# Kernel tuning notes

Hardware: AMD Instinct MI355X
Metric: run time of the kernel (lower is better)

Reference implementation:

```python
import jax, jax.numpy as jnp
import numpy as np
import math

B, T, C = 4, 2048, 1024
NH, D = 16, 64  # n_head, head_dim; NH * D == C


def setup_inputs() -> dict:
    key = jax.random.key(0)
    ks = jax.random.split(key, 7)
    std = 0.02
    return {
        "x": jax.random.normal(ks[0], (B, T, C), dtype=jnp.float32),
        "W_attn": jax.random.normal(ks[1], (C, 3 * C), dtype=jnp.float32) * std,
        "b_attn": jax.random.normal(ks[2], (3 * C,), dtype=jnp.float32) * std,
        "bQ": jax.random.normal(ks[3], (NH, D), dtype=jnp.float32) * 0.1 + 0.5,
        "bK": jax.random.normal(ks[4], (NH, D), dtype=jnp.float32) * 0.1 + 0.3,
        "W_proj": jax.random.normal(ks[5], (C, C), dtype=jnp.float32) * std,
        "b_proj": jax.random.normal(ks[6], (C,), dtype=jnp.float32) * std,
    }


def reference(x, W_attn, b_attn, bQ, bK, W_proj, b_proj):
    Bx, Tx, Cx = x.shape
    qkv = x @ W_attn + b_attn                      # [B, T, 3C]
    q, k, v = jnp.split(qkv, 3, axis=2)
    # [B, T, C] -> [B, NH, T, D]
    q = q.reshape(Bx, Tx, NH, D).transpose(0, 2, 1, 3)
    k = k.reshape(Bx, Tx, NH, D).transpose(0, 2, 1, 3)
    v = v.reshape(Bx, Tx, NH, D).transpose(0, 2, 1, 3)
    # per-head disorder bias added to Q and K before the dot product
    q = q + bQ[None, :, None, :]
    k = k + bK[None, :, None, :]
    scores = jnp.einsum('bhqd,bhkd->bhqk', q, k) / math.sqrt(D)  # [B, NH, T, T]
    causal = jnp.tril(jnp.ones((Tx, Tx), dtype=bool))
    scores = jnp.where(causal[None, None], scores, jnp.float32(-jnp.inf))
    att = jax.nn.softmax(scores, axis=-1)
    y = jnp.einsum('bhqk,bhkd->bhqd', att, v)      # [B, NH, T, D]
    y = y.transpose(0, 2, 1, 3).reshape(Bx, Tx, Cx)
    return y @ W_proj + b_proj
```

## Files before the change

### kernel.cpp

```cpp
#include <hip/hip_runtime.h>

typedef unsigned short u16;
typedef unsigned int u32;
typedef __bf16 bf16x8 __attribute__((ext_vector_type(8)));
typedef float f32x4 __attribute__((ext_vector_type(4)));

#define B_  4
#define T_  2048
#define C_  1024
#define NH_ 16
#define D_  64
#define M_  (B_*T_)
#define N_QKV (3*C_)

#define ATTN_BLOCKS 1024

#define BARRIER()  __asm__ __volatile__("s_barrier" ::: "memory")
#define WAIT_VM4() __asm__ __volatile__("s_waitcnt vmcnt(4)" ::: "memory")
#define WAIT_VM0() __asm__ __volatile__("s_waitcnt vmcnt(0)" ::: "memory")

__device__ __forceinline__ void async_copy16(void* lds, const void* gptr) {
  __builtin_amdgcn_global_load_lds(
      (const __attribute__((address_space(1))) u32*)gptr,
      (__attribute__((address_space(3))) u32*)(u32)(uintptr_t)lds,
      16, 0, 0);
}

__device__ __forceinline__ u16 f2bf(float f) {
  union { float f; unsigned u; } c; c.f = f;
  unsigned u = c.u;
  unsigned r = (u + 0x7fffu + ((u >> 16) & 1u)) >> 16;
  return (u16)r;
}

__global__ __launch_bounds__(256) void conv_bf16(const float* __restrict__ in,
                                                 u16* __restrict__ out, int n) {
  int i = (blockIdx.x * 256 + threadIdx.x) * 4;
  if (i < n) {
    float4 f = *reinterpret_cast<const float4*>(in + i);
    u16 o[4] = { f2bf(f.x), f2bf(f.y), f2bf(f.z), f2bf(f.w) };
    *reinterpret_cast<uint2*>(out + i) = *reinterpret_cast<uint2*>(o);
  }
}

__global__ __launch_bounds__(256) void transpose_bf16(const float* __restrict__ in,
                                                      u16* __restrict__ out,
                                                      int K, int N) {
  __shared__ float tile[32][33];
  int bi = blockIdx.y;
  int bj = blockIdx.x;
  int tx = threadIdx.x & 31;
  int ty = threadIdx.x >> 5;
#pragma unroll
  for (int i = 0; i < 4; ++i) {
    int row = ty + i * 8;
    tile[row][tx] = in[(bi * 32 + row) * N + bj * 32 + tx];
  }
  __syncthreads();
#pragma unroll
  for (int i = 0; i < 4; ++i) {
    int row = ty + i * 8;
    out[(bj * 32 + row) * K + bi * 32 + tx] = f2bf(tile[tx][row]);
  }
}

__global__ __launch_bounds__(256) void gemm_qkv(const u16* __restrict__ A,
                                                const u16* __restrict__ Bt,
                                                const float* __restrict__ b_attn,
                                                const float* __restrict__ bQ,
                                                const float* __restrict__ bK,
                                                u16* __restrict__ qo,
                                                u16* __restrict__ ko,
                                                u16* __restrict__ vo) {
  const int K = C_;
  int bm = blockIdx.y, bn = blockIdx.x;
  int tid = threadIdx.x;
  int wid = tid >> 6, lane = tid & 63;
  int lm = lane & 15, lq = lane >> 4;
  int wm = (wid >> 1) * 64, wn = (wid & 1) * 64;

  __shared__ u16 As[128 * 32];
  __shared__ u16 Bs[128 * 32];

  f32x4 acc[4][4];
#pragma unroll
  for (int i = 0; i < 4; ++i)
#pragma unroll
    for (int j = 0; j < 4; ++j) acc[i][j] = (f32x4){0.f, 0.f, 0.f, 0.f};

  const u16* Ab = A + (bm * 128) * K;
  const u16* Bb = Bt + (bn * 128) * K;
  int srow = lane >> 2;
  int scol = (lane & 3) * 8;

  for (int k0 = 0; k0 < K; k0 += 32) {
    __syncthreads();
#pragma unroll
    for (int j = 0; j < 2; ++j) {
      int c = wid * 2 + j;
      int row = c * 16 + srow;
      async_copy16(&As[c * 512], Ab + row * K + k0 + scol);
      async_copy16(&Bs[c * 512], Bb + row * K + k0 + scol);
    }
    __syncthreads();
    bf16x8 af[4], bf[4];
#pragma unroll
    for (int mt = 0; mt < 4; ++mt)
      af[mt] = *reinterpret_cast<const bf16x8*>(&As[(wm + mt * 16 + lm) * 32 + lq * 8]);
#pragma unroll
    for (int nt = 0; nt < 4; ++nt)
      bf[nt] = *reinterpret_cast<const bf16x8*>(&Bs[(wn + nt * 16 + lm) * 32 + lq * 8]);
#pragma unroll
    for (int mt = 0; mt < 4; ++mt)
#pragma unroll
      for (int nt = 0; nt < 4; ++nt)
        acc[mt][nt] = __builtin_amdgcn_mfma_f32_16x16x32_bf16(af[mt], bf[nt], acc[mt][nt], 0, 0, 0);
  }

  const float qscale = 0.18033688011112042f;
#pragma unroll
  for (int mt = 0; mt < 4; ++mt) {
#pragma unroll
    for (int nt = 0; nt < 4; ++nt) {
#pragma unroll
      for (int r = 0; r < 4; ++r) {
        int m = bm * 128 + wm + mt * 16 + lq * 4 + r;
        int n = bn * 128 + wn + nt * 16 + lm;
        float val = acc[mt][nt][r] + b_attn[n];
        int sel = n >> 10;
        int c = n & 1023;
        int h = c >> 6;
        int d = c & 63;
        int b = m >> 11;
        int t = m & 2047;
        if (sel == 0)      qo[(((b * NH_ + h) * T_) + t) * D_ + d] = f2bf((val + bQ[c]) * qscale);
        else if (sel == 1) ko[(((b * NH_ + h) * T_) + t) * D_ + d] = f2bf(val + bK[c]);
        else               vo[(((b * NH_ + h) * D_) + d) * T_ + t] = f2bf(val);
      }
    }
  }
}

__global__ __launch_bounds__(256, 4) void attn_kernel(const u16* __restrict__ q,
                                                      const u16* __restrict__ k,
                                                      const u16* __restrict__ vt,
                                                      u16* __restrict__ y) {
  int tid = threadIdx.x;
  int w = tid >> 6, lane = tid & 63;
  int lm = lane & 15, lq = lane >> 4;

  __shared__ u16 Ks[2][64 * 64];
  __shared__ u16 Vs[2][64 * 64];

  int srow = lane >> 3;
  int sg   = (lane & 7) ^ srow;

  int idx = blockIdx.x;
  int c8 = idx & 255, jq = idx >> 8;
  int a = c8 & 7, gq = c8 >> 3;
  int qt, bh;
  if (jq == 0)      { qt = 15 - a; bh = gq; }
  else if (jq == 1) { qt = 8 + a;  bh = 32 + gq; }
  else if (jq == 2) { qt = 7 - a;  bh = gq; }
  else              { qt = a;      bh = 32 + gq; }

  int b = bh >> 4, h = bh & 15;
  const int klast = 2 * qt + 1;
  const int qrow0 = qt * 128 + w * 32;

  const u16* qb = q + ((size_t)bh * T_ + qrow0) * D_;
  const u16* kb = k + (size_t)bh * T_ * D_;
  const u16* vb = vt + (size_t)bh * D_ * T_;

  auto stage_K = [&](int buf, int kbi) {
    const u16* gb = kb + (size_t)(kbi * 64) * 64;
#pragma unroll
    for (int j = 0; j < 2; ++j) {
      int c = w * 2 + j;
      async_copy16(&Ks[buf][c * 512], gb + (c * 8 + srow) * 64 + sg * 8);
    }
  };
  auto stage_V = [&](int buf, int kbi) {
    const u16* gb = vb + kbi * 64;
#pragma unroll
    for (int j = 0; j < 2; ++j) {
      int c = w * 2 + j;
      async_copy16(&Vs[buf][c * 512], gb + (size_t)(c * 8 + srow) * T_ + sg * 8);
    }
  };

  bf16x8 bq[2][2];
#pragma unroll
  for (int qt2 = 0; qt2 < 2; ++qt2) {
    const u16* qp = qb + (qt2 * 16 + lm) * D_ + lq * 8;
    bq[qt2][0] = *reinterpret_cast<const bf16x8*>(qp);
    bq[qt2][1] = *reinterpret_cast<const bf16x8*>(qp + 32);
  }

  f32x4 o[4][2];
#pragma unroll
  for (int dt = 0; dt < 4; ++dt)
#pragma unroll
    for (int qt2 = 0; qt2 < 2; ++qt2) o[dt][qt2] = (f32x4){0.f, 0.f, 0.f, 0.f};
  float mprev[2] = {-1e30f, -1e30f}, lsum[2] = {0.f, 0.f};

  stage_K(0, 0); stage_V(0, 0);
  stage_K(1, 1); stage_V(1, 1);

  for (int kbi = 0; kbi <= klast; ++kbi) {
    int buf = kbi & 1;
    WAIT_VM4();
    BARRIER();

    bf16x8 kf[4][2];
#pragma unroll
    for (int kt = 0; kt < 4; ++kt) {
      const u16* base = &Ks[buf][(kt * 16 + lm) * 64];
      kf[kt][0] = *reinterpret_cast<const bf16x8*>(base + ((lq ^ (lm & 7)) * 8));
      kf[kt][1] = *reinterpret_cast<const bf16x8*>(base + (((4 + lq) ^ (lm & 7)) * 8));
    }

    f32x4 s[4][2];
#pragma unroll
    for (int kt = 0; kt < 4; ++kt)
#pragma unroll
      for (int qt2 = 0; qt2 < 2; ++qt2) {
        f32x4 z = (f32x4){0.f, 0.f, 0.f, 0.f};
        z = __builtin_amdgcn_mfma_f32_16x16x32_bf16(kf[kt][0], bq[qt2][0], z, 0, 0, 0);
        z = __builtin_amdgcn_mfma_f32_16x16x32_bf16(kf[kt][1], bq[qt2][1], z, 0, 0, 0);
        s[kt][qt2] = z;
      }

    bool maskt = (kbi * 64 + 63 > qrow0);
    bf16x8 pb[2][2];
#pragma unroll
    for (int qt2 = 0; qt2 < 2; ++qt2) {
      int qg = qrow0 + qt2 * 16 + lm;
      if (maskt) {
#pragma unroll
        for (int kt = 0; kt < 4; ++kt)
#pragma unroll
          for (int r = 0; r < 4; ++r) {
            int key = kbi * 64 + kt * 16 + lq * 4 + r;
            if (key > qg) s[kt][qt2][r] = -1e30f;
          }
      }
      float mx[4];
#pragma unroll
      for (int kt = 0; kt < 4; ++kt)
        mx[kt] = fmaxf(fmaxf(s[kt][qt2][0], s[kt][qt2][1]),
                       fmaxf(s[kt][qt2][2], s[kt][qt2][3]));
      float mval = fmaxf(fmaxf(mx[0], mx[1]), fmaxf(mx[2], mx[3]));
      mval = fmaxf(mval, __shfl_xor(mval, 16));
      mval = fmaxf(mval, __shfl_xor(mval, 32));
      float mold = mprev[qt2];
      float mnew = fmaxf(mold, mval);
      unsigned long long upd = __ballot(mval > mold);
      if (upd) {
        float alpha = __builtin_exp2f(mold - mnew);
        lsum[qt2] *= alpha;
#pragma unroll
        for (int dt = 0; dt < 4; ++dt) o[dt][qt2] *= alpha;
        mprev[qt2] = mnew;
      }
      float rs = 0.f;
      unsigned pw[8];
#pragma unroll
      for (int kt = 0; kt < 4; ++kt) {
        unsigned pu[4];
#pragma unroll
        for (int r = 0; r < 4; ++r) {
          float p = __builtin_exp2f(s[kt][qt2][r] - mnew);
          rs += p;
          union { float f; unsigned u; } cc; cc.f = p;
          pu[r] = cc.u;
        }
        pw[kt * 2]     = __builtin_amdgcn_perm(pu[1], pu[0], 0x07060302u);
        pw[kt * 2 + 1] = __builtin_amdgcn_perm(pu[3], pu[2], 0x07060302u);
      }
      rs += __shfl_xor(rs, 16);
      rs += __shfl_xor(rs, 32);
      lsum[qt2] += rs;
      union { unsigned u[4]; bf16x8 v; } b0, b1;
#pragma unroll
      for (int t = 0; t < 4; ++t) { b0.u[t] = pw[t]; b1.u[t] = pw[4 + t]; }
      pb[qt2][0] = b0.v;
      pb[qt2][1] = b1.v;
    }

    {
      int r7 = lm & 7;
      int h4 = (lq & 1) * 4;
      int g0 = lq >> 1;
#pragma unroll
      for (int dt = 0; dt < 4; ++dt) {
        const u16* vbase = &Vs[buf][(dt * 16 + lm) * 64];
        union { unsigned long long qd[2]; bf16x8 v; } t0, t1;
        t0.qd[0] = *reinterpret_cast<const unsigned long long*>(vbase + ((g0 ^ r7) * 8) + h4);
        t0.qd[1] = *reinterpret_cast<const unsigned long long*>(vbase + (((g0 + 2) ^ r7) * 8) + h4);
        t1.qd[0] = *reinterpret_cast<const unsigned long long*>(vbase + (((g0 + 4) ^ r7) * 8) + h4);
        t1.qd[1] = *reinterpret_cast<const unsigned long long*>(vbase + (((g0 + 6) ^ r7) * 8) + h4);
#pragma unroll
        for (int qt2 = 0; qt2 < 2; ++qt2) {
          o[dt][qt2] = __builtin_amdgcn_mfma_f32_16x16x32_bf16(t0.v, pb[qt2][0], o[dt][qt2], 0, 0, 0);
          o[dt][qt2] = __builtin_amdgcn_mfma_f32_16x16x32_bf16(t1.v, pb[qt2][1], o[dt][qt2], 0, 0, 0);
        }
      }
    }

    BARRIER();
    int nk = (kbi + 2 <= klast) ? kbi + 2 : klast;
    stage_K(buf, nk); stage_V(buf, nk);
  }

  WAIT_VM0();

#pragma unroll
  for (int qt2 = 0; qt2 < 2; ++qt2) {
    float inv = 1.f / lsum[qt2];
    int qg = qrow0 + qt2 * 16 + lm;
#pragma unroll
    for (int dt = 0; dt < 4; ++dt) {
      u16 wb[4];
#pragma unroll
      for (int r = 0; r < 4; ++r) wb[r] = f2bf(o[dt][qt2][r] * inv);
      int d = dt * 16 + lq * 4;
      *reinterpret_cast<uint2*>(&y[((size_t)(b * T_ + qg) * NH_ + h) * D_ + d]) =
          *reinterpret_cast<uint2*>(wb);
    }
  }
}

__global__ __launch_bounds__(256) void gemm_proj(const u16* __restrict__ A,
                                                 const u16* __restrict__ Bt,
                                                 const float* __restrict__ b_proj,
                                                 float* __restrict__ out) {
  const int K = C_, N = C_;
  int bm = blockIdx.y, bn = blockIdx.x;
  int tid = threadIdx.x;
  int wid = tid >> 6, lane = tid & 63;
  int lm = lane & 15, lq = lane >> 4;
  int wm = (wid >> 1) * 64, wn = (wid & 1) * 64;

  __shared__ u16 As[128 * 32];
  __shared__ u16 Bs[128 * 32];

  f32x4 acc[4][4];
#pragma unroll
  for (int i = 0; i < 4; ++i)
#pragma unroll
    for (int j = 0; j < 4; ++j) acc[i][j] = (f32x4){0.f, 0.f, 0.f, 0.f};

  const u16* Ab = A + (bm * 128) * K;
  const u16* Bb = Bt + (bn * 128) * K;
  int srow = lane >> 2;
  int scol = (lane & 3) * 8;

  for (int k0 = 0; k0 < K; k0 += 32) {
    __syncthreads();
#pragma unroll
    for (int j = 0; j < 2; ++j) {
      int c = wid * 2 + j;
      int row = c * 16 + srow;
      async_copy16(&As[c * 512], Ab + row * K + k0 + scol);
      async_copy16(&Bs[c * 512], Bb + row * K + k0 + scol);
    }
    __syncthreads();
    bf16x8 af[4], bf[4];
#pragma unroll
    for (int mt = 0; mt < 4; ++mt)
      af[mt] = *reinterpret_cast<const bf16x8*>(&As[(wm + mt * 16 + lm) * 32 + lq * 8]);
#pragma unroll
    for (int nt = 0; nt < 4; ++nt)
      bf[nt] = *reinterpret_cast<const bf16x8*>(&Bs[(wn + nt * 16 + lm) * 32 + lq * 8]);
#pragma unroll
    for (int mt = 0; mt < 4; ++mt)
#pragma unroll
      for (int nt = 0; nt < 4; ++nt)
        acc[mt][nt] = __builtin_amdgcn_mfma_f32_16x16x32_bf16(af[mt], bf[nt], acc[mt][nt], 0, 0, 0);
  }

#pragma unroll
  for (int mt = 0; mt < 4; ++mt) {
#pragma unroll
    for (int nt = 0; nt < 4; ++nt) {
#pragma unroll
      for (int r = 0; r < 4; ++r) {
        int m = bm * 128 + wm + mt * 16 + lq * 4 + r;
        int n = bn * 128 + wn + nt * 16 + lm;
        out[m * N + n] = acc[mt][nt][r] + b_proj[n];
      }
    }
  }
}

extern "C" void kernel_launch(void* const* d_in, const int* in_sizes, int n_in,
                              void* d_out, int out_size, void* d_ws, size_t ws_size,
                              hipStream_t stream) {
  const float* x      = (const float*)d_in[0];
  const float* W_attn = (const float*)d_in[1];
  const float* b_attn = (const float*)d_in[2];
  const float* bQ     = (const float*)d_in[3];
  const float* bK     = (const float*)d_in[4];
  const float* W_proj = (const float*)d_in[5];
  const float* b_proj = (const float*)d_in[6];
  float* out = (float*)d_out;

  char* ws = (char*)d_ws;
  u16* xb  = (u16*)(ws);
  u16* WaT = (u16*)(ws + 16777216);
  u16* WpT = (u16*)(ws + 23068672);
  u16* qw  = (u16*)(ws + 25165824);
  u16* kw  = (u16*)(ws + 41943040);
  u16* vw  = (u16*)(ws + 58720256);
  u16* yw  = (u16*)(ws + 75497472);

  conv_bf16<<<M_ * C_ / (4 * 256), 256, 0, stream>>>(x, xb, M_ * C_);
  {
    dim3 g(N_QKV / 32, C_ / 32);
    transpose_bf16<<<g, 256, 0, stream>>>(W_attn, WaT, C_, N_QKV);
  }
  {
    dim3 g(C_ / 32, C_ / 32);
    transpose_bf16<<<g, 256, 0, stream>>>(W_proj, WpT, C_, C_);
  }
  {
    dim3 g(N_QKV / 128, M_ / 128);
    gemm_qkv<<<g, 256, 0, stream>>>(xb, WaT, b_attn, bQ, bK, qw, kw, vw);
  }
  attn_kernel<<<ATTN_BLOCKS, 256, 0, stream>>>(qw, kw, vw, yw);
  {
    dim3 g(C_ / 128, M_ / 128);
    gemm_proj<<<g, 256, 0, stream>>>(yw, WpT, b_proj, out);
  }
}
```

Measured before the change: 317.0 us.

## Rewrite QKV GEMM as 256x256 double-buffered pipelined tile; double-buffer proj GEMM

Rebuilds the QKV projection GEMM around 256x256 output tiles with 512 threads, a K-step of 64, XOR-swizzled LDS layout, double-buffered async global-to-LDS loads interleaved with MFMA quads, s_setprio hints, and an XCD-aware block remap. It also vectorizes the V-transpose stores. The output projection GEMM gets a simple double-buffered prefetch that replaces its two syncthreads per K-step. The aim is to hide global load latency and raise MFMA utilization, at the cost of much larger LDS use (128KB for QKV), heavier register pressure, and fragile manual waitcnt and barrier ordering.

```diff
diff --git a/kernel.cpp b/kernel.cpp
--- a/kernel.cpp
+++ b/kernel.cpp
@@ -18,6 +18,7 @@
 #define BARRIER()  __asm__ __volatile__("s_barrier" ::: "memory")
 #define WAIT_VM4() __asm__ __volatile__("s_waitcnt vmcnt(4)" ::: "memory")
 #define WAIT_VM0() __asm__ __volatile__("s_waitcnt vmcnt(0)" ::: "memory")
+#define LGKM0()    __asm__ __volatile__("s_waitcnt lgkmcnt(0)" ::: "memory")
 
 __device__ __forceinline__ void async_copy16(void* lds, const void* gptr) {
   __builtin_amdgcn_global_load_lds(
@@ -64,78 +65,151 @@
   }
 }
 
-__global__ __launch_bounds__(256) void gemm_qkv(const u16* __restrict__ A,
-                                                const u16* __restrict__ Bt,
-                                                const float* __restrict__ b_attn,
-                                                const float* __restrict__ bQ,
-                                                const float* __restrict__ bK,
-                                                u16* __restrict__ qo,
-                                                u16* __restrict__ ko,
-                                                u16* __restrict__ vo) {
+__global__ __launch_bounds__(512, 2) void gemm_qkv(const u16* __restrict__ A,
+                                                   const u16* __restrict__ Bt,
+                                                   const float* __restrict__ b_attn,
+                                                   const float* __restrict__ bQ,
+                                                   const float* __restrict__ bK,
+                                                   u16* __restrict__ qo,
+                                                   u16* __restrict__ ko,
+                                                   u16* __restrict__ vo) {
   const int K = C_;
-  int bm = blockIdx.y, bn = blockIdx.x;
+  const int NT = K / 64;
+  int bid = blockIdx.x;
+  int wg = (bid & 7) * 48 + (bid >> 3);
+  int bm = wg / 12, bn = wg % 12;
+
   int tid = threadIdx.x;
-  int wid = tid >> 6, lane = tid & 63;
+  int w = tid >> 6, lane = tid & 63;
   int lm = lane & 15, lq = lane >> 4;
-  int wm = (wid >> 1) * 64, wn = (wid & 1) * 64;
-
-  __shared__ u16 As[128 * 32];
-  __shared__ u16 Bs[128 * 32];
-
-  f32x4 acc[4][4];
-#pragma unroll
-  for (int i = 0; i < 4; ++i)
+  int wr = w >> 2, wc = w & 3;
+
+  __shared__ u16 As[2][256 * 64];
+  __shared__ u16 Bs[2][256 * 64];
+
+  const u16* Ab = A + (size_t)(bm * 256) * K;
+  const u16* Bb = Bt + (size_t)(bn * 256) * K;
+  int srow = lane >> 3;
+  int sgc  = ((lane & 7) ^ srow) * 8;
+
+  auto stageA = [&](int bb, int h, int t) {
+#pragma unroll
+    for (int j = 0; j < 2; ++j)
+      async_copy16(&As[bb][h * 8192 + j * 4096 + w * 512],
+                   Ab + (size_t)(h * 128 + j * 64 + w * 8 + srow) * K + t * 64 + sgc);
+  };
+  auto stageB = [&](int bb, int h, int t) {
+#pragma unroll
+    for (int j = 0; j < 2; ++j)
+      async_copy16(&Bs[bb][h * 8192 + j * 4096 + w * 512],
+                   Bb + (size_t)(h * 128 + j * 64 + w * 8 + srow) * K + t * 64 + sgc);
+  };
+
+  f32x4 acc[8][4];
+#pragma unroll
+  for (int i = 0; i < 8; ++i)
 #pragma unroll
     for (int j = 0; j < 4; ++j) acc[i][j] = (f32x4){0.f, 0.f, 0.f, 0.f};
 
-  const u16* Ab = A + (bm * 128) * K;
-  const u16* Bb = Bt + (bn * 128) * K;
-  int srow = lane >> 2;
-  int scol = (lane & 3) * 8;
-
-  for (int k0 = 0; k0 < K; k0 += 32) {
-    __syncthreads();
-#pragma unroll
-    for (int j = 0; j < 2; ++j) {
-      int c = wid * 2 + j;
-      int row = c * 16 + srow;
-      async_copy16(&As[c * 512], Ab + row * K + k0 + scol);
-      async_copy16(&Bs[c * 512], Bb + row * K + k0 + scol);
-    }
-    __syncthreads();
-    bf16x8 af[4], bf[4];
-#pragma unroll
-    for (int mt = 0; mt < 4; ++mt)
-      af[mt] = *reinterpret_cast<const bf16x8*>(&As[(wm + mt * 16 + lm) * 32 + lq * 8]);
-#pragma unroll
-    for (int nt = 0; nt < 4; ++nt)
-      bf[nt] = *reinterpret_cast<const bf16x8*>(&Bs[(wn + nt * 16 + lm) * 32 + lq * 8]);
-#pragma unroll
-    for (int mt = 0; mt < 4; ++mt)
-#pragma unroll
-      for (int nt = 0; nt < 4; ++nt)
-        acc[mt][nt] = __builtin_amdgcn_mfma_f32_16x16x32_bf16(af[mt], bf[nt], acc[mt][nt], 0, 0, 0);
-  }
+  auto readA4 = [&](bf16x8 (&af)[4][2], int bb, int mh) {
+#pragma unroll
+    for (int mf = 0; mf < 4; ++mf) {
+      const u16* base = &As[bb][(wr * 128 + (mh * 4 + mf) * 16 + lm) * 64];
+#pragma unroll
+      for (int kh = 0; kh < 2; ++kh)
+        af[mf][kh] = *reinterpret_cast<const bf16x8*>(base + (((kh * 4 + lq) ^ (lm & 7)) * 8));
+    }
+  };
+  auto readB8 = [&](bf16x8 (&bf)[4][2], int bb) {
+#pragma unroll
+    for (int nf = 0; nf < 4; ++nf) {
+      const u16* base = &Bs[bb][(wc * 64 + nf * 16 + lm) * 64];
+#pragma unroll
+      for (int kh = 0; kh < 2; ++kh)
+        bf[nf][kh] = *reinterpret_cast<const bf16x8*>(base + (((kh * 4 + lq) ^ (lm & 7)) * 8));
+    }
+  };
+  auto quad = [&](bf16x8 (&af)[4][2], bf16x8 (&bf)[4][2], int mb, int nb) {
+#pragma unroll
+    for (int mf = 0; mf < 4; ++mf)
+#pragma unroll
+      for (int nf = 0; nf < 2; ++nf)
+#pragma unroll
+        for (int kh = 0; kh < 2; ++kh)
+          acc[mb + mf][nb + nf] = __builtin_amdgcn_mfma_f32_16x16x32_bf16(
+              af[mf][kh], bf[nb + nf][kh], acc[mb + mf][nb + nf], 0, 0, 0);
+  };
+
+  auto process = [&](int bb, int tbx, int bbx, int tay, int bay) {
+    bf16x8 bfr[4][2], aflo[4][2], afhi[4][2];
+    readB8(bfr, bb);
+    readA4(aflo, bb, 0);
+    stageB(bbx, 0, tbx);
+    BARRIER(); LGKM0();
+    __builtin_amdgcn_s_setprio(1); quad(aflo, bfr, 0, 0); __builtin_amdgcn_s_setprio(0);
+    BARRIER();
+    readA4(afhi, bb, 1);
+    stageB(bbx, 1, tbx);
+    BARRIER(); LGKM0();
+    __builtin_amdgcn_s_setprio(1); quad(aflo, bfr, 0, 2); __builtin_amdgcn_s_setprio(0);
+    BARRIER();
+    stageA(bay, 0, tay);
+    BARRIER();
+    __builtin_amdgcn_s_setprio(1); quad(afhi, bfr, 4, 0); __builtin_amdgcn_s_setprio(0);
+    BARRIER();
+    stageA(bay, 1, tay);
+    WAIT_VM4();
+    BARRIER();
+    __builtin_amdgcn_s_setprio(1); quad(afhi, bfr, 4, 2); __builtin_amdgcn_s_setprio(0);
+    BARRIER();
+  };
+
+  stageA(0, 0, 0); stageA(0, 1, 0); stageB(0, 0, 0); stageB(0, 1, 0);
+  stageA(1, 0, 1); stageA(1, 1, 1);
+  WAIT_VM4();
+  BARRIER();
+
+  for (int i = 0; i < NT / 2; ++i) {
+    int t0 = 2 * i, t1 = t0 + 1;
+    int s2 = (t0 + 2 < NT) ? t0 + 2 : NT - 1;
+    int s3 = (t0 + 3 < NT) ? t0 + 3 : NT - 1;
+    process(0, t1, 1, s2, 0);
+    process(1, s2, 0, s3, 1);
+  }
+  WAIT_VM0();
 
   const float qscale = 0.18033688011112042f;
-#pragma unroll
-  for (int mt = 0; mt < 4; ++mt) {
-#pragma unroll
-    for (int nt = 0; nt < 4; ++nt) {
-#pragma unroll
-      for (int r = 0; r < 4; ++r) {
-        int m = bm * 128 + wm + mt * 16 + lq * 4 + r;
-        int n = bn * 128 + wn + nt * 16 + lm;
-        float val = acc[mt][nt][r] + b_attn[n];
-        int sel = n >> 10;
-        int c = n & 1023;
-        int h = c >> 6;
-        int d = c & 63;
-        int b = m >> 11;
-        int t = m & 2047;
-        if (sel == 0)      qo[(((b * NH_ + h) * T_) + t) * D_ + d] = f2bf((val + bQ[c]) * qscale);
-        else if (sel == 1) ko[(((b * NH_ + h) * T_) + t) * D_ + d] = f2bf(val + bK[c]);
-        else               vo[(((b * NH_ + h) * D_) + d) * T_ + t] = f2bf(val);
+  int sel = bn >> 2;
+#pragma unroll
+  for (int mf = 0; mf < 8; ++mf) {
+#pragma unroll
+    for (int nf = 0; nf < 4; ++nf) {
+      int n = bn * 256 + wc * 64 + nf * 16 + lm;
+      float bias = b_attn[n];
+      int c = n & 1023;
+      int h = c >> 6;
+      int d = c & 63;
+      int m0 = bm * 256 + wr * 128 + mf * 16 + lq * 4;
+      int b = m0 >> 11;
+      int t = m0 & 2047;
+      if (sel == 0) {
+        float qb = bQ[c];
+#pragma unroll
+        for (int r = 0; r < 4; ++r)
+          qo[(((size_t)(b * NH_ + h) * T_) + t + r) * D_ + d] =
+              f2bf((acc[mf][nf][r] + bias + qb) * qscale);
+      } else if (sel == 1) {
+        float kb2 = bK[c];
+#pragma unroll
+        for (int r = 0; r < 4; ++r)
+          ko[(((size_t)(b * NH_ + h) * T_) + t + r) * D_ + d] =
+              f2bf(acc[mf][nf][r] + bias + kb2);
+      } else {
+        u16 wb[4];
+#pragma unroll
+        for (int r = 0; r < 4; ++r) wb[r] = f2bf(acc[mf][nf][r] + bias);
+        *reinterpret_cast<uint2*>(&vo[((size_t)(b * NH_ + h) * D_ + d) * T_ + t]) =
+            *reinterpret_cast<uint2*>(wb);
       }
     }
   }
@@ -342,8 +416,8 @@
   int lm = lane & 15, lq = lane >> 4;
   int wm = (wid >> 1) * 64, wn = (wid & 1) * 64;
 
-  __shared__ u16 As[128 * 32];
-  __shared__ u16 Bs[128 * 32];
+  __shared__ u16 As[2][128 * 32];
+  __shared__ u16 Bs[2][128 * 32];
 
   f32x4 acc[4][4];
 #pragma unroll
@@ -356,29 +430,40 @@
   int srow = lane >> 2;
   int scol = (lane & 3) * 8;
 
-  for (int k0 = 0; k0 < K; k0 += 32) {
-    __syncthreads();
+  auto stage = [&](int bb, int k0) {
 #pragma unroll
     for (int j = 0; j < 2; ++j) {
       int c = wid * 2 + j;
       int row = c * 16 + srow;
-      async_copy16(&As[c * 512], Ab + row * K + k0 + scol);
-      async_copy16(&Bs[c * 512], Bb + row * K + k0 + scol);
-    }
-    __syncthreads();
+      async_copy16(&As[bb][c * 512], Ab + row * K + k0 + scol);
+      async_copy16(&Bs[bb][c * 512], Bb + row * K + k0 + scol);
+    }
+  };
+
+  stage(0, 0);
+  const int NTp = K / 32;
+  for (int t = 0; t < NTp; ++t) {
+    int bb = t & 1;
+    int k1 = (t + 1 < NTp) ? (t + 1) * 32 : t * 32;
+    stage(bb ^ 1, k1);
+    WAIT_VM4();
+    BARRIER();
     bf16x8 af[4], bf[4];
 #pragma unroll
     for (int mt = 0; mt < 4; ++mt)
-      af[mt] = *reinterpret_cast<const bf16x8*>(&As[(wm + mt * 16 + lm) * 32 + lq * 8]);
+      af[mt] = *reinterpret_cast<const bf16x8*>(&As[bb][(wm + mt * 16 + lm) * 32 + lq * 8]);
 #pragma unroll
     for (int nt = 0; nt < 4; ++nt)
-      bf[nt] = *reinterpret_cast<const bf16x8*>(&Bs[(wn + nt * 16 + lm) * 32 + lq * 8]);
+      bf[nt] = *reinterpret_cast<const bf16x8*>(&Bs[bb][(wn + nt * 16 + lm) * 32 + lq * 8]);
 #pragma unroll
     for (int mt = 0; mt < 4; ++mt)
 #pragma unroll
       for (int nt = 0; nt < 4; ++nt)
         acc[mt][nt] = __builtin_amdgcn_mfma_f32_16x16x32_bf16(af[mt], bf[nt], acc[mt][nt], 0, 0, 0);
-  }
+    LGKM0();
+    BARRIER();
+  }
+  WAIT_VM0();
 
 #pragma unroll
   for (int mt = 0; mt < 4; ++mt) {
@@ -424,10 +509,7 @@
     dim3 g(C_ / 32, C_ / 32);
     transpose_bf16<<<g, 256, 0, stream>>>(W_proj, WpT, C_, C_);
   }
-  {
-    dim3 g(N_QKV / 128, M_ / 128);
-    gemm_qkv<<<g, 256, 0, stream>>>(xb, WaT, b_attn, bQ, bK, qw, kw, vw);
-  }
+  gemm_qkv<<<(M_ / 256) * (N_QKV / 256), 512, 0, stream>>>(xb, WaT, b_attn, bQ, bK, qw, kw, vw);
   attn_kernel<<<ATTN_BLOCKS, 256, 0, stream>>>(qw, kw, vw, yw);
   {
     dim3 g(C_ / 128, M_ / 128);
```

New measurement: 313.9 us. No clear change (-1.0%).
